# Kernel tuning notes

Hardware: AMD Instinct MI355X
Metric: run time of the kernel (lower is better)

Reference implementation:

```python
import jax, jax.numpy as jnp
import numpy as np

NUM_HEADS = 8  # from init_kwargs

def _conv1x1(x, W, b):
    # x: [B, Cin, H, W], W: [Cout, Cin], b: [Cout]  (nn.Conv2d kernel_size=1)
    return jnp.einsum('bchw,oc->bohw', x, W) + b[None, :, None, None]

def setup_inputs() -> dict:
    key = jax.random.key(0)
    ks = jax.random.split(key, 9)
    B, C, H, W = 8, 256, 32, 32
    Ck, Cv, Co = 256, 256, 256
    s = 1.0 / np.sqrt(C)
    return {
        'x':  jax.random.normal(ks[0], (B, C, H, W), dtype=jnp.float32),
        'Wq': jax.random.normal(ks[1], (Ck, C), dtype=jnp.float32) * s,
        'bq': jax.random.normal(ks[2], (Ck,), dtype=jnp.float32) * 0.02,
        'Wk': jax.random.normal(ks[3], (Ck, C), dtype=jnp.float32) * s,
        'bk': jax.random.normal(ks[4], (Ck,), dtype=jnp.float32) * 0.02,
        'Wv': jax.random.normal(ks[5], (Cv, C), dtype=jnp.float32) * s,
        'bv': jax.random.normal(ks[6], (Cv,), dtype=jnp.float32) * 0.02,
        'Wo': jax.random.normal(ks[7], (Co, Cv), dtype=jnp.float32) * s,
        'bo': jax.random.normal(ks[8], (Co,), dtype=jnp.float32) * 0.02,
    }

def reference(x, Wq, bq, Wk, bk, Wv, bv, Wo, bo):
    B, C, H, W = x.shape
    q = _conv1x1(x, Wq, bq)  # [B, Ck, H, W]
    k = _conv1x1(x, Wk, bk)  # [B, Ck, H, W]
    v = _conv1x1(x, Wv, bv)  # [B, Cv, H, W]
    nh = NUM_HEADS
    dk = q.shape[1] // nh
    dv = v.shape[1] // nh
    N = H * W
    # split heads, flatten spatial dims into sequence
    q = q.reshape(B, nh, dk, N) * (dk ** -0.5)
    k = k.reshape(B, nh, dk, N)
    v = v.reshape(B, nh, dv, N)
    logits = jnp.einsum('bhdn,bhdm->bhnm', q, k)        # [B, nh, N, N]
    attn = jax.nn.softmax(logits, axis=-1)
    o = jnp.einsum('bhnm,bhdm->bhdn', attn, v)           # [B, nh, dv, N]
    o = o.reshape(B, nh * dv, H, W)
    return _conv1x1(o, Wo, bo)                           # [B, Co, H, W]
```

## Files before the change

kernel.cpp:

```cpp
#include <hip/hip_runtime.h>
#include <math.h>

typedef unsigned short u16;
typedef __attribute__((ext_vector_type(8))) unsigned short u16x8;
typedef __attribute__((ext_vector_type(8))) short s16x8;
typedef __attribute__((ext_vector_type(4))) float f32x4;

#define QK_SCALE (0.17677669529663687f * 1.4426950408889634f)

__device__ __forceinline__ unsigned cvt2(float lo, float hi) {
  unsigned r;
  asm("v_cvt_pk_bf16_f32 %0, %1, %2" : "=v"(r) : "v"(lo), "v"(hi));
  return r;
}
__device__ __forceinline__ u16 f2bf(float f) { return (u16)cvt2(f, f); }
__device__ __forceinline__ u16x8 ld16(const void* p) { u16x8 v; __builtin_memcpy(&v, p, 16); return v; }
__device__ __forceinline__ void st16(void* p, u16x8 v) { __builtin_memcpy(p, &v, 16); }
__device__ __forceinline__ void st16s(void* p, s16x8 v) { __builtin_memcpy(p, &v, 16); }
__device__ __forceinline__ void st4(void* p, unsigned v) { __builtin_memcpy(p, &v, 4); }
__device__ __forceinline__ f32x4 ldf4(const void* p) { f32x4 v; __builtin_memcpy(&v, p, 16); return v; }
__device__ __forceinline__ void stf4(void* p, f32x4 v) { __builtin_memcpy(p, &v, 16); }
__device__ __forceinline__ s16x8 frag16(const void* p) { s16x8 v; __builtin_memcpy(&v, p, 16); return v; }
__device__ __forceinline__ s16x8 pack8(f32x4 lo, f32x4 hi) {
  union { unsigned u[4]; s16x8 s; } c;
  c.u[0] = cvt2(lo.x, lo.y); c.u[1] = cvt2(lo.z, lo.w);
  c.u[2] = cvt2(hi.x, hi.y); c.u[3] = cvt2(hi.z, hi.w);
  return c.s;
}

__global__ __launch_bounds__(256) void r19_qkv(
    const float* __restrict__ x,
    const float* __restrict__ Wq, const float* __restrict__ bq,
    const float* __restrict__ Wk, const float* __restrict__ bk,
    const float* __restrict__ Wv, const float* __restrict__ bv,
    u16* __restrict__ qo, u16* __restrict__ ko, u16* __restrict__ vo)
{
  __shared__ u16 xt[64][264];
  __shared__ u16 wlds[192][40];

  const int t = threadIdx.x;
  const int ntile = blockIdx.x, hp = blockIdx.y, b = blockIdx.z;
  const int n0 = ntile * 64, h0 = hp * 2;
  const int w = t >> 6, lane = t & 63, l15 = lane & 15, quad = lane >> 4;

  {
    const float* xrow = x + ((size_t)b * 256 + t) * 1024 + n0;
#pragma unroll
    for (int i = 0; i < 64; i += 4) {
      const f32x4 a = ldf4(xrow + i);
      xt[i + 0][t] = f2bf(a.x); xt[i + 1][t] = f2bf(a.y);
      xt[i + 2][t] = f2bf(a.z); xt[i + 3][t] = f2bf(a.w);
    }
  }

  f32x4 acc[12];
#pragma unroll
  for (int i = 0; i < 12; ++i) acc[i] = (f32x4){0.f, 0.f, 0.f, 0.f};

  for (int ks = 0; ks < 8; ++ks) {
    __syncthreads();
    if (t < 192) {
      const int m = t >> 6, hh = (t >> 5) & 1, r = t & 31;
      const float* M = (m == 0) ? Wq : (m == 1) ? Wk : Wv;
      const float* src = M + (size_t)((h0 + hh) * 32 + r) * 256 + ks * 32;
      st16s(&wlds[t][0],  pack8(ldf4(src),      ldf4(src + 4)));
      st16s(&wlds[t][8],  pack8(ldf4(src + 8),  ldf4(src + 12)));
      st16s(&wlds[t][16], pack8(ldf4(src + 16), ldf4(src + 20)));
      st16s(&wlds[t][24], pack8(ldf4(src + 24), ldf4(src + 28)));
    }
    __syncthreads();

    const s16x8 bfrag = frag16(&xt[w * 16 + l15][ks * 32 + quad * 8]);
#pragma unroll
    for (int mt = 0; mt < 12; ++mt) {
      const s16x8 af = frag16(&wlds[mt * 16 + l15][quad * 8]);
      acc[mt] = __builtin_amdgcn_mfma_f32_16x16x32_bf16(af, bfrag, acc[mt], 0, 0, 0);
    }
  }

  const int n = n0 + w * 16 + l15;
  const int sig = n & 127;
  const int ntn = sig >> 4, q4 = (sig >> 2) & 3, rn = sig & 3;
  const int nperm = (n & ~127) | ((ntn >> 1) << 5) | (q4 << 3) | ((ntn & 1) << 2) | rn;
#pragma unroll
  for (int hh = 0; hh < 2; ++hh) {
    const int h = h0 + hh;
    const size_t bh = (size_t)(b * 8 + h);
    u16* qrow = qo + (bh * 1024 + n) * 32;
    u16* krow = ko + (bh * 1024 + n) * 32;
#pragma unroll
    for (int half = 0; half < 2; ++half) {
      const int d0 = half * 16 + quad * 4;
      const f32x4 aq = acc[hh * 2 + half];
      const f32x4 ak = acc[4 + hh * 2 + half];
      const f32x4 av = acc[8 + hh * 2 + half];
      st4(qrow + d0,     cvt2((aq.x + bq[h * 32 + d0 + 0]) * QK_SCALE,
                              (aq.y + bq[h * 32 + d0 + 1]) * QK_SCALE));
      st4(qrow + d0 + 2, cvt2((aq.z + bq[h * 32 + d0 + 2]) * QK_SCALE,
                              (aq.w + bq[h * 32 + d0 + 3]) * QK_SCALE));
      st4(krow + d0,     cvt2(ak.x + bk[h * 32 + d0 + 0],
                              ak.y + bk[h * 32 + d0 + 1]));
      st4(krow + d0 + 2, cvt2(ak.z + bk[h * 32 + d0 + 2],
                              ak.w + bk[h * 32 + d0 + 3]));
#pragma unroll
      for (int rr = 0; rr < 4; ++rr) {
        const int d = d0 + rr;
        vo[(bh * 32 + d) * 1024 + nperm] = f2bf(av[rr] + bv[h * 32 + d]);
      }
    }
  }
}

__global__ __launch_bounds__(256) void r19_attn(
    const u16* __restrict__ qw, const u16* __restrict__ kw,
    const u16* __restrict__ vw, float* __restrict__ out)
{
  __shared__ u16 klds[128][40];
  __shared__ u16 vlds[32][136];

  const int t = threadIdx.x;
  const int qtile = blockIdx.x;
  const int bh = blockIdx.y;
  const int w = t >> 6, lane = t & 63, l15 = lane & 15, quad = lane >> 4;

  const s16x8 qfrag = frag16(
      qw + ((size_t)bh * 1024 + qtile * 64 + w * 16 + l15) * 32 + quad * 8);

  const u16* kbase = kw + ((size_t)bh * 1024 + (t >> 1)) * 32 + (t & 1) * 16;
  const u16* vbase = vw + ((size_t)bh * 32 + (t >> 3)) * 1024 + (t & 7) * 16;

  u16x8 gk0 = ld16(kbase), gk1 = ld16(kbase + 8);
  u16x8 gv0 = ld16(vbase), gv1 = ld16(vbase + 8);

  f32x4 o0 = {0.f, 0.f, 0.f, 0.f}, o1 = {0.f, 0.f, 0.f, 0.f};
  float mrun = -1e30f, lrun = 0.f;

  for (int kb = 0; kb < 8; ++kb) {
    if (kb) __syncthreads();
    st16(&klds[t >> 1][(t & 1) * 16], gk0);
    st16(&klds[t >> 1][(t & 1) * 16 + 8], gk1);
    st16(&vlds[t >> 3][(t & 7) * 16], gv0);
    st16(&vlds[t >> 3][(t & 7) * 16 + 8], gv1);
    if (kb < 7) {
      const u16* kn = kbase + (size_t)(kb + 1) * (128 * 32);
      const u16* vn = vbase + (size_t)(kb + 1) * 128;
      gk0 = ld16(kn); gk1 = ld16(kn + 8);
      gv0 = ld16(vn); gv1 = ld16(vn + 8);
    }
    __syncthreads();

    f32x4 s[8];
    const f32x4 zz = {0.f, 0.f, 0.f, 0.f};
#pragma unroll
    for (int nt2 = 0; nt2 < 8; ++nt2) {
      const s16x8 kf = frag16(&klds[nt2 * 16 + l15][quad * 8]);
      s[nt2] = __builtin_amdgcn_mfma_f32_16x16x32_bf16(kf, qfrag, zz, 0, 0, 0);
    }

    float mx = fmaxf(fmaxf(s[0][0], s[0][1]), fmaxf(s[0][2], s[0][3]));
#pragma unroll
    for (int nt2 = 1; nt2 < 8; ++nt2)
      mx = fmaxf(mx, fmaxf(fmaxf(s[nt2][0], s[nt2][1]),
                           fmaxf(s[nt2][2], s[nt2][3])));
    mx = fmaxf(mx, __shfl_xor(mx, 16));
    mx = fmaxf(mx, __shfl_xor(mx, 32));
    const float mnew = fmaxf(mrun, mx);
    const float alpha = exp2f(mrun - mnew);
    float rs = 0.f;
#pragma unroll
    for (int nt2 = 0; nt2 < 8; ++nt2) {
#pragma unroll
      for (int r = 0; r < 4; ++r) {
        s[nt2][r] = exp2f(s[nt2][r] - mnew);
        rs += s[nt2][r];
      }
    }
    rs += __shfl_xor(rs, 16);
    rs += __shfl_xor(rs, 32);
    lrun = lrun * alpha + rs;
    mrun = mnew;
#pragma unroll
    for (int r = 0; r < 4; ++r) { o0[r] *= alpha; o1[r] *= alpha; }

#pragma unroll
    for (int ks = 0; ks < 4; ++ks) {
      const s16x8 pf  = pack8(s[2 * ks], s[2 * ks + 1]);
      const s16x8 vf0 = frag16(&vlds[l15][ks * 32 + quad * 8]);
      const s16x8 vf1 = frag16(&vlds[16 + l15][ks * 32 + quad * 8]);
      o0 = __builtin_amdgcn_mfma_f32_16x16x32_bf16(vf0, pf, o0, 0, 0, 0);
      o1 = __builtin_amdgcn_mfma_f32_16x16x32_bf16(vf1, pf, o1, 0, 0, 0);
    }
  }

  const float inv = 1.0f / lrun;
  const int b = bh >> 3, hh = bh & 7;
  float* obase = out + ((size_t)b * 256 + hh * 32) * 1024
               + qtile * 64 + w * 16 + l15;
#pragma unroll
  for (int r = 0; r < 4; ++r) {
    obase[(size_t)(quad * 4 + r) * 1024]      = o0[r] * inv;
    obase[(size_t)(16 + quad * 4 + r) * 1024] = o1[r] * inv;
  }
}

__global__ __launch_bounds__(256) void r19_oproj(
    const float* __restrict__ Wo, const float* __restrict__ bo,
    float* __restrict__ out)
{
  __shared__ u16 o2t[32][264];
  const int t = threadIdx.x;
  const int nt = blockIdx.x, b = blockIdx.y;
  const int w = t >> 6, lane = t & 63, l15 = lane & 15, quad = lane >> 4;

  {
    const float* src = out + ((size_t)b * 256 + t) * 1024 + nt * 32;
#pragma unroll
    for (int i = 0; i < 32; i += 4) {
      const f32x4 a = ldf4(src + i);
      o2t[i + 0][t] = f2bf(a.x); o2t[i + 1][t] = f2bf(a.y);
      o2t[i + 2][t] = f2bf(a.z); o2t[i + 3][t] = f2bf(a.w);
    }
  }
  __syncthreads();

  f32x4 acc[4][2];
#pragma unroll
  for (int mt = 0; mt < 4; ++mt) {
    acc[mt][0] = (f32x4){0.f, 0.f, 0.f, 0.f};
    acc[mt][1] = (f32x4){0.f, 0.f, 0.f, 0.f};
  }

  for (int ks = 0; ks < 8; ++ks) {
    const s16x8 b0 = frag16(&o2t[l15][ks * 32 + quad * 8]);
    const s16x8 b1 = frag16(&o2t[16 + l15][ks * 32 + quad * 8]);
#pragma unroll
    for (int mt = 0; mt < 4; ++mt) {
      const float* wsrc = Wo + (size_t)(w * 64 + mt * 16 + l15) * 256 + ks * 32 + quad * 8;
      const s16x8 af = pack8(ldf4(wsrc), ldf4(wsrc + 4));
      acc[mt][0] = __builtin_amdgcn_mfma_f32_16x16x32_bf16(af, b0, acc[mt][0], 0, 0, 0);
      acc[mt][1] = __builtin_amdgcn_mfma_f32_16x16x32_bf16(af, b1, acc[mt][1], 0, 0, 0);
    }
  }

#pragma unroll
  for (int mt = 0; mt < 4; ++mt) {
#pragma unroll
    for (int r = 0; r < 4; ++r) {
      const int oc = w * 64 + mt * 16 + quad * 4 + r;
      const float bov = bo[oc];
      out[((size_t)b * 256 + oc) * 1024 + nt * 32 + l15]      = acc[mt][0][r] + bov;
      out[((size_t)b * 256 + oc) * 1024 + nt * 32 + 16 + l15] = acc[mt][1][r] + bov;
    }
  }
}

extern "C" void kernel_launch(void* const* d_in, const int* in_sizes, int n_in,
                              void* d_out, int out_size, void* d_ws, size_t ws_size,
                              hipStream_t stream) {
  (void)in_sizes; (void)n_in; (void)out_size; (void)ws_size;
  const float* x  = (const float*)d_in[0];
  const float* Wq = (const float*)d_in[1];
  const float* bq = (const float*)d_in[2];
  const float* Wk = (const float*)d_in[3];
  const float* bk = (const float*)d_in[4];
  const float* Wv = (const float*)d_in[5];
  const float* bv = (const float*)d_in[6];
  const float* Wo = (const float*)d_in[7];
  const float* bo = (const float*)d_in[8];
  float* out = (float*)d_out;

  char* ws = (char*)d_ws;
  u16* qw = (u16*)(ws);
  u16* kw = (u16*)(ws + (4u << 20));
  u16* vw = (u16*)(ws + (8u << 20));

  r19_qkv<<<dim3(16, 4, 8), 256, 0, stream>>>(
      x, Wq, bq, Wk, bk, Wv, bv, qw, kw, vw);
  r19_attn<<<dim3(16, 64), 256, 0, stream>>>(qw, kw, vw, out);
  r19_oproj<<<dim3(32, 8), 256, 0, stream>>>(Wo, bo, out);
}
```

Before: 137.5 us.

## Split keys across warps in attention and merge partial softmax via LDS

Restructures the attention kernel so each warp processes all 64 queries of the tile over its own quarter of the keys, reading K and V fragments directly from global memory instead of staging them through LDS with per-tile barriers. Partial max, sum and output accumulators are then combined across warps through shared memory. This is meant to remove the LDS staging and synchronisation overhead and to reuse each K/V fragment across four query tiles. In exchange it raises register usage and relies on cache-served direct global fragment loads.

Result: slower. 178.1 us (+29.6%).

```diff
diff --git a/kernel.cpp b/kernel.cpp
--- a/kernel.cpp
+++ b/kernel.cpp
@@ -28,7 +28,7 @@
   return c.s;
 }
 
-__global__ __launch_bounds__(256) void r19_qkv(
+__global__ __launch_bounds__(256) void r21_qkv(
     const float* __restrict__ x,
     const float* __restrict__ Wq, const float* __restrict__ bq,
     const float* __restrict__ Wk, const float* __restrict__ bk,
@@ -91,7 +91,7 @@
 #pragma unroll
     for (int half = 0; half < 2; ++half) {
       const int d0 = half * 16 + quad * 4;
-      const f32x4 aq = acc[hh * 2 + half];
+      const f32x4 aq = acc[0 + hh * 2 + half];
       const f32x4 ak = acc[4 + hh * 2 + half];
       const f32x4 av = acc[8 + hh * 2 + half];
       st4(qrow + d0,     cvt2((aq.x + bq[h * 32 + d0 + 0]) * QK_SCALE,
@@ -111,99 +111,135 @@
   }
 }
 
-__global__ __launch_bounds__(256) void r19_attn(
+__global__ __launch_bounds__(256) void r21_attn(
     const u16* __restrict__ qw, const u16* __restrict__ kw,
     const u16* __restrict__ vw, float* __restrict__ out)
 {
-  __shared__ u16 klds[128][40];
-  __shared__ u16 vlds[32][136];
+  __shared__ float olds[4][64][36];
+  __shared__ float mlm[4][4][16];
+  __shared__ float mll[4][4][16];
 
   const int t = threadIdx.x;
   const int qtile = blockIdx.x;
   const int bh = blockIdx.y;
   const int w = t >> 6, lane = t & 63, l15 = lane & 15, quad = lane >> 4;
 
-  const s16x8 qfrag = frag16(
-      qw + ((size_t)bh * 1024 + qtile * 64 + w * 16 + l15) * 32 + quad * 8);
-
-  const u16* kbase = kw + ((size_t)bh * 1024 + (t >> 1)) * 32 + (t & 1) * 16;
-  const u16* vbase = vw + ((size_t)bh * 32 + (t >> 3)) * 1024 + (t & 7) * 16;
-
-  u16x8 gk0 = ld16(kbase), gk1 = ld16(kbase + 8);
-  u16x8 gv0 = ld16(vbase), gv1 = ld16(vbase + 8);
-
-  f32x4 o0 = {0.f, 0.f, 0.f, 0.f}, o1 = {0.f, 0.f, 0.f, 0.f};
-  float mrun = -1e30f, lrun = 0.f;
-
-  for (int kb = 0; kb < 8; ++kb) {
-    if (kb) __syncthreads();
-    st16(&klds[t >> 1][(t & 1) * 16], gk0);
-    st16(&klds[t >> 1][(t & 1) * 16 + 8], gk1);
-    st16(&vlds[t >> 3][(t & 7) * 16], gv0);
-    st16(&vlds[t >> 3][(t & 7) * 16 + 8], gv1);
-    if (kb < 7) {
-      const u16* kn = kbase + (size_t)(kb + 1) * (128 * 32);
-      const u16* vn = vbase + (size_t)(kb + 1) * 128;
-      gk0 = ld16(kn); gk1 = ld16(kn + 8);
-      gv0 = ld16(vn); gv1 = ld16(vn + 8);
-    }
-    __syncthreads();
-
-    f32x4 s[8];
-    const f32x4 zz = {0.f, 0.f, 0.f, 0.f};
-#pragma unroll
-    for (int nt2 = 0; nt2 < 8; ++nt2) {
-      const s16x8 kf = frag16(&klds[nt2 * 16 + l15][quad * 8]);
-      s[nt2] = __builtin_amdgcn_mfma_f32_16x16x32_bf16(kf, qfrag, zz, 0, 0, 0);
-    }
-
-    float mx = fmaxf(fmaxf(s[0][0], s[0][1]), fmaxf(s[0][2], s[0][3]));
-#pragma unroll
-    for (int nt2 = 1; nt2 < 8; ++nt2)
-      mx = fmaxf(mx, fmaxf(fmaxf(s[nt2][0], s[nt2][1]),
-                           fmaxf(s[nt2][2], s[nt2][3])));
-    mx = fmaxf(mx, __shfl_xor(mx, 16));
-    mx = fmaxf(mx, __shfl_xor(mx, 32));
-    const float mnew = fmaxf(mrun, mx);
-    const float alpha = exp2f(mrun - mnew);
-    float rs = 0.f;
-#pragma unroll
-    for (int nt2 = 0; nt2 < 8; ++nt2) {
-#pragma unroll
-      for (int r = 0; r < 4; ++r) {
-        s[nt2][r] = exp2f(s[nt2][r] - mnew);
-        rs += s[nt2][r];
+  s16x8 qfrag[4];
+#pragma unroll
+  for (int qs = 0; qs < 4; ++qs)
+    qfrag[qs] = frag16(
+        qw + ((size_t)bh * 1024 + qtile * 64 + qs * 16 + l15) * 32 + quad * 8);
+
+  const u16* kwb = kw + (size_t)bh * 1024 * 32;
+  const u16* vwb = vw + (size_t)bh * 32 * 1024;
+
+  f32x4 o[4][2];
+#pragma unroll
+  for (int qs = 0; qs < 4; ++qs) {
+    o[qs][0] = (f32x4){0.f, 0.f, 0.f, 0.f};
+    o[qs][1] = (f32x4){0.f, 0.f, 0.f, 0.f};
+  }
+  float m[4] = {-1e30f, -1e30f, -1e30f, -1e30f};
+  float l[4] = {0.f, 0.f, 0.f, 0.f};
+
+  const f32x4 zz = {0.f, 0.f, 0.f, 0.f};
+#pragma unroll
+  for (int c = 0; c < 4; ++c) {
+    const int cb = w * 64 + c * 256;
+    const u16* kp = kwb + (size_t)cb * 32;
+    const u16* vp = vwb + cb;
+
+    f32x4 s[4][4];
+#pragma unroll
+    for (int kt = 0; kt < 4; ++kt) {
+      const s16x8 kf = frag16(kp + (size_t)(kt * 16 + l15) * 32 + quad * 8);
+#pragma unroll
+      for (int qs = 0; qs < 4; ++qs)
+        s[qs][kt] = __builtin_amdgcn_mfma_f32_16x16x32_bf16(kf, qfrag[qs], zz, 0, 0, 0);
+    }
+
+#pragma unroll
+    for (int qs = 0; qs < 4; ++qs) {
+      float mx = fmaxf(fmaxf(s[qs][0][0], s[qs][0][1]),
+                       fmaxf(s[qs][0][2], s[qs][0][3]));
+#pragma unroll
+      for (int kt = 1; kt < 4; ++kt)
+        mx = fmaxf(mx, fmaxf(fmaxf(s[qs][kt][0], s[qs][kt][1]),
+                             fmaxf(s[qs][kt][2], s[qs][kt][3])));
+      mx = fmaxf(mx, __shfl_xor(mx, 16));
+      mx = fmaxf(mx, __shfl_xor(mx, 32));
+      const float mnew = fmaxf(m[qs], mx);
+      const float al = exp2f(m[qs] - mnew);
+      float rs = 0.f;
+#pragma unroll
+      for (int kt = 0; kt < 4; ++kt) {
+#pragma unroll
+        for (int r = 0; r < 4; ++r) {
+          s[qs][kt][r] = exp2f(s[qs][kt][r] - mnew);
+          rs += s[qs][kt][r];
+        }
       }
-    }
-    rs += __shfl_xor(rs, 16);
-    rs += __shfl_xor(rs, 32);
-    lrun = lrun * alpha + rs;
-    mrun = mnew;
-#pragma unroll
-    for (int r = 0; r < 4; ++r) { o0[r] *= alpha; o1[r] *= alpha; }
-
-#pragma unroll
-    for (int ks = 0; ks < 4; ++ks) {
-      const s16x8 pf  = pack8(s[2 * ks], s[2 * ks + 1]);
-      const s16x8 vf0 = frag16(&vlds[l15][ks * 32 + quad * 8]);
-      const s16x8 vf1 = frag16(&vlds[16 + l15][ks * 32 + quad * 8]);
-      o0 = __builtin_amdgcn_mfma_f32_16x16x32_bf16(vf0, pf, o0, 0, 0, 0);
-      o1 = __builtin_amdgcn_mfma_f32_16x16x32_bf16(vf1, pf, o1, 0, 0, 0);
-    }
-  }
-
-  const float inv = 1.0f / lrun;
+      rs += __shfl_xor(rs, 16);
+      rs += __shfl_xor(rs, 32);
+      l[qs] = l[qs] * al + rs;
+      m[qs] = mnew;
+#pragma unroll
+      for (int r = 0; r < 4; ++r) { o[qs][0][r] *= al; o[qs][1][r] *= al; }
+    }
+
+#pragma unroll
+    for (int ks2 = 0; ks2 < 2; ++ks2) {
+      const s16x8 vf0 = frag16(vp + (size_t)l15 * 1024 + ks2 * 32 + quad * 8);
+      const s16x8 vf1 = frag16(vp + (size_t)(16 + l15) * 1024 + ks2 * 32 + quad * 8);
+#pragma unroll
+      for (int qs = 0; qs < 4; ++qs) {
+        const s16x8 pf = pack8(s[qs][2 * ks2], s[qs][2 * ks2 + 1]);
+        o[qs][0] = __builtin_amdgcn_mfma_f32_16x16x32_bf16(vf0, pf, o[qs][0], 0, 0, 0);
+        o[qs][1] = __builtin_amdgcn_mfma_f32_16x16x32_bf16(vf1, pf, o[qs][1], 0, 0, 0);
+      }
+    }
+  }
+
+  mlm[w][quad][l15] = m[quad];
+  mll[w][quad][l15] = l[quad];
+  __syncthreads();
+#pragma unroll
+  for (int qs = 0; qs < 4; ++qs) {
+    float mv0 = mlm[0][qs][l15], mv1 = mlm[1][qs][l15];
+    float mv2 = mlm[2][qs][l15], mv3 = mlm[3][qs][l15];
+    const float M = fmaxf(fmaxf(mv0, mv1), fmaxf(mv2, mv3));
+    const float L = exp2f(mv0 - M) * mll[0][qs][l15]
+                  + exp2f(mv1 - M) * mll[1][qs][l15]
+                  + exp2f(mv2 - M) * mll[2][qs][l15]
+                  + exp2f(mv3 - M) * mll[3][qs][l15];
+    const float sc = exp2f(m[qs] - M) / L;
+    f32x4 a0, a1;
+#pragma unroll
+    for (int r = 0; r < 4; ++r) { a0[r] = o[qs][0][r] * sc; a1[r] = o[qs][1][r] * sc; }
+    stf4(&olds[w][qs * 16 + l15][quad * 4], a0);
+    stf4(&olds[w][qs * 16 + l15][16 + quad * 4], a1);
+  }
+  __syncthreads();
+
+  f32x4 r0 = {0.f, 0.f, 0.f, 0.f}, r1 = {0.f, 0.f, 0.f, 0.f};
+#pragma unroll
+  for (int wv = 0; wv < 4; ++wv) {
+    const f32x4 p0 = ldf4(&olds[wv][w * 16 + l15][quad * 4]);
+    const f32x4 p1 = ldf4(&olds[wv][w * 16 + l15][16 + quad * 4]);
+#pragma unroll
+    for (int r = 0; r < 4; ++r) { r0[r] += p0[r]; r1[r] += p1[r]; }
+  }
   const int b = bh >> 3, hh = bh & 7;
   float* obase = out + ((size_t)b * 256 + hh * 32) * 1024
                + qtile * 64 + w * 16 + l15;
 #pragma unroll
   for (int r = 0; r < 4; ++r) {
-    obase[(size_t)(quad * 4 + r) * 1024]      = o0[r] * inv;
-    obase[(size_t)(16 + quad * 4 + r) * 1024] = o1[r] * inv;
-  }
-}
-
-__global__ __launch_bounds__(256) void r19_oproj(
+    obase[(size_t)(quad * 4 + r) * 1024]      = r0[r];
+    obase[(size_t)(16 + quad * 4 + r) * 1024] = r1[r];
+  }
+}
+
+__global__ __launch_bounds__(256) void r21_oproj(
     const float* __restrict__ Wo, const float* __restrict__ bo,
     float* __restrict__ out)
 {
@@ -274,8 +310,8 @@
   u16* kw = (u16*)(ws + (4u << 20));
   u16* vw = (u16*)(ws + (8u << 20));
 
-  r19_qkv<<<dim3(16, 4, 8), 256, 0, stream>>>(
+  r21_qkv<<<dim3(16, 4, 8), 256, 0, stream>>>(
       x, Wq, bq, Wk, bk, Wv, bv, qw, kw, vw);
-  r19_attn<<<dim3(16, 64), 256, 0, stream>>>(qw, kw, vw, out);
-  r19_oproj<<<dim3(32, 8), 256, 0, stream>>>(Wo, bo, out);
-}
+  r21_attn<<<dim3(16, 64), 256, 0, stream>>>(qw, kw, vw, out);
+  r21_oproj<<<dim3(32, 8), 256, 0, stream>>>(Wo, bo, out);
+}
```

## Coalesce x/W staging loads, swizzle LDS, double-buffer Wo in oproj

Applied to the files above, without the earlier changes.

The QKV and output-projection kernels now load activations and weights with coalesced lanes, where each thread previously walked its own row. The transposed bf16 tiles in LDS use an XOR swizzle to avoid bank conflicts. In the output projection, Wo is staged into double-buffered LDS instead of being read and converted from global memory separately by each wave. This cuts strided global traffic and duplicated weight loads, at the cost of more LDS use (lower occupancy) and an extra barrier per k-step.

New measurement: 132.4 us. 3.7% less time.

```diff
diff --git a/kernel.cpp b/kernel.cpp
--- a/kernel.cpp
+++ b/kernel.cpp
@@ -18,6 +18,10 @@
 __device__ __forceinline__ void st16(void* p, u16x8 v) { __builtin_memcpy(p, &v, 16); }
 __device__ __forceinline__ void st16s(void* p, s16x8 v) { __builtin_memcpy(p, &v, 16); }
 __device__ __forceinline__ void st4(void* p, unsigned v) { __builtin_memcpy(p, &v, 4); }
+__device__ __forceinline__ void st8(void* p, unsigned lo, unsigned hi) {
+  unsigned long long v = ((unsigned long long)hi << 32) | (unsigned long long)lo;
+  __builtin_memcpy(p, &v, 8);
+}
 __device__ __forceinline__ f32x4 ldf4(const void* p) { f32x4 v; __builtin_memcpy(&v, p, 16); return v; }
 __device__ __forceinline__ void stf4(void* p, f32x4 v) { __builtin_memcpy(p, &v, 16); }
 __device__ __forceinline__ s16x8 frag16(const void* p) { s16x8 v; __builtin_memcpy(&v, p, 16); return v; }
@@ -28,7 +32,7 @@
   return c.s;
 }
 
-__global__ __launch_bounds__(256) void r19_qkv(
+__global__ __launch_bounds__(256) void r22_qkv(
     const float* __restrict__ x,
     const float* __restrict__ Wq, const float* __restrict__ bq,
     const float* __restrict__ Wk, const float* __restrict__ bk,
@@ -42,14 +46,19 @@
   const int ntile = blockIdx.x, hp = blockIdx.y, b = blockIdx.z;
   const int n0 = ntile * 64, h0 = hp * 2;
   const int w = t >> 6, lane = t & 63, l15 = lane & 15, quad = lane >> 4;
+  const int oct = t & 7;
 
   {
-    const float* xrow = x + ((size_t)b * 256 + t) * 1024 + n0;
-#pragma unroll
-    for (int i = 0; i < 64; i += 4) {
-      const f32x4 a = ldf4(xrow + i);
-      xt[i + 0][t] = f2bf(a.x); xt[i + 1][t] = f2bf(a.y);
-      xt[i + 2][t] = f2bf(a.z); xt[i + 3][t] = f2bf(a.w);
+    const int i = t & 15, co = t >> 4;
+    const float* xb = x + ((size_t)b * 256 + co) * 1024 + n0 + i * 4;
+    const int msk = (i & 7) << 3;
+#pragma unroll
+    for (int p = 0; p < 16; ++p) {
+      const f32x4 a = ldf4(xb + (size_t)p * 16 * 1024);
+      const int c = p * 16 + co;
+#pragma unroll
+      for (int j = 0; j < 4; ++j)
+        xt[i * 4 + j][(c ^ msk)] = f2bf(a[j]);
     }
   }
 
@@ -59,18 +68,22 @@
 
   for (int ks = 0; ks < 8; ++ks) {
     __syncthreads();
-    if (t < 192) {
-      const int m = t >> 6, hh = (t >> 5) & 1, r = t & 31;
-      const float* M = (m == 0) ? Wq : (m == 1) ? Wk : Wv;
-      const float* src = M + (size_t)((h0 + hh) * 32 + r) * 256 + ks * 32;
-      st16s(&wlds[t][0],  pack8(ldf4(src),      ldf4(src + 4)));
-      st16s(&wlds[t][8],  pack8(ldf4(src + 8),  ldf4(src + 12)));
-      st16s(&wlds[t][16], pack8(ldf4(src + 16), ldf4(src + 20)));
-      st16s(&wlds[t][24], pack8(ldf4(src + 24), ldf4(src + 28)));
+    {
+#pragma unroll
+      for (int u = 0; u < 6; ++u) {
+        const int row = (u * 256 + t) >> 3;
+        const int m = row >> 6, hh = (row >> 5) & 1, rr = row & 31;
+        const float* M = (m == 0) ? Wq : (m == 1) ? Wk : Wv;
+        const f32x4 a = ldf4(M + (size_t)((h0 + hh) * 32 + rr) * 256
+                             + ks * 32 + oct * 4);
+        st8(&wlds[row][oct * 4], cvt2(a.x, a.y), cvt2(a.z, a.w));
+      }
     }
     __syncthreads();
 
-    const s16x8 bfrag = frag16(&xt[w * 16 + l15][ks * 32 + quad * 8]);
+    const int nrow = w * 16 + l15;
+    const s16x8 bfrag = frag16(
+        &xt[nrow][(ks * 32 + quad * 8) ^ (((nrow >> 2) & 7) << 3)]);
 #pragma unroll
     for (int mt = 0; mt < 12; ++mt) {
       const s16x8 af = frag16(&wlds[mt * 16 + l15][quad * 8]);
@@ -91,7 +104,7 @@
 #pragma unroll
     for (int half = 0; half < 2; ++half) {
       const int d0 = half * 16 + quad * 4;
-      const f32x4 aq = acc[hh * 2 + half];
+      const f32x4 aq = acc[0 + hh * 2 + half];
       const f32x4 ak = acc[4 + hh * 2 + half];
       const f32x4 av = acc[8 + hh * 2 + half];
       st4(qrow + d0,     cvt2((aq.x + bq[h * 32 + d0 + 0]) * QK_SCALE,
@@ -111,7 +124,7 @@
   }
 }
 
-__global__ __launch_bounds__(256) void r19_attn(
+__global__ __launch_bounds__(256) void r22_attn(
     const u16* __restrict__ qw, const u16* __restrict__ kw,
     const u16* __restrict__ vw, float* __restrict__ out)
 {
@@ -203,24 +216,42 @@
   }
 }
 
-__global__ __launch_bounds__(256) void r19_oproj(
+__global__ __launch_bounds__(256) void r22_oproj(
     const float* __restrict__ Wo, const float* __restrict__ bo,
     float* __restrict__ out)
 {
   __shared__ u16 o2t[32][264];
+  __shared__ u16 wl3[2][256][40];
+
   const int t = threadIdx.x;
   const int nt = blockIdx.x, b = blockIdx.y;
   const int w = t >> 6, lane = t & 63, l15 = lane & 15, quad = lane >> 4;
+  const int oct = t & 7;
 
   {
-    const float* src = out + ((size_t)b * 256 + t) * 1024 + nt * 32;
-#pragma unroll
-    for (int i = 0; i < 32; i += 4) {
-      const f32x4 a = ldf4(src + i);
-      o2t[i + 0][t] = f2bf(a.x); o2t[i + 1][t] = f2bf(a.y);
-      o2t[i + 2][t] = f2bf(a.z); o2t[i + 3][t] = f2bf(a.w);
-    }
-  }
+    const int co = t >> 3;
+    const float* ob = out + ((size_t)b * 256 + co) * 1024 + nt * 32 + oct * 4;
+    const int msk = oct << 3;
+#pragma unroll
+    for (int p = 0; p < 8; ++p) {
+      const f32x4 a = ldf4(ob + (size_t)p * 32 * 1024);
+      const int c = p * 32 + co;
+#pragma unroll
+      for (int j = 0; j < 4; ++j)
+        o2t[oct * 4 + j][(c ^ msk)] = f2bf(a[j]);
+    }
+  }
+
+  auto stage_wo = [&](int ks, int buf) {
+#pragma unroll
+    for (int u = 0; u < 8; ++u) {
+      const int row = u * 32 + (t >> 3);
+      const f32x4 a = ldf4(Wo + (size_t)row * 256 + ks * 32 + oct * 4);
+      st8(&wl3[buf][row][oct * 4], cvt2(a.x, a.y), cvt2(a.z, a.w));
+    }
+  };
+
+  stage_wo(0, 0);
   __syncthreads();
 
   f32x4 acc[4][2];
@@ -231,15 +262,18 @@
   }
 
   for (int ks = 0; ks < 8; ++ks) {
-    const s16x8 b0 = frag16(&o2t[l15][ks * 32 + quad * 8]);
-    const s16x8 b1 = frag16(&o2t[16 + l15][ks * 32 + quad * 8]);
+    if (ks < 7) stage_wo(ks + 1, (ks + 1) & 1);
+    const s16x8 b0 = frag16(
+        &o2t[l15][(ks * 32 + quad * 8) ^ (((l15 >> 2) & 7) << 3)]);
+    const s16x8 b1 = frag16(
+        &o2t[16 + l15][(ks * 32 + quad * 8) ^ ((((16 + l15) >> 2) & 7) << 3)]);
 #pragma unroll
     for (int mt = 0; mt < 4; ++mt) {
-      const float* wsrc = Wo + (size_t)(w * 64 + mt * 16 + l15) * 256 + ks * 32 + quad * 8;
-      const s16x8 af = pack8(ldf4(wsrc), ldf4(wsrc + 4));
+      const s16x8 af = frag16(&wl3[ks & 1][w * 64 + mt * 16 + l15][quad * 8]);
       acc[mt][0] = __builtin_amdgcn_mfma_f32_16x16x32_bf16(af, b0, acc[mt][0], 0, 0, 0);
       acc[mt][1] = __builtin_amdgcn_mfma_f32_16x16x32_bf16(af, b1, acc[mt][1], 0, 0, 0);
     }
+    __syncthreads();
   }
 
 #pragma unroll
@@ -274,8 +308,8 @@
   u16* kw = (u16*)(ws + (4u << 20));
   u16* vw = (u16*)(ws + (8u << 20));
 
-  r19_qkv<<<dim3(16, 4, 8), 256, 0, stream>>>(
+  r22_qkv<<<dim3(16, 4, 8), 256, 0, stream>>>(
       x, Wq, bq, Wk, bk, Wv, bv, qw, kw, vw);
-  r19_attn<<<dim3(16, 64), 256, 0, stream>>>(qw, kw, vw, out);
-  r19_oproj<<<dim3(32, 8), 256, 0, stream>>>(Wo, bo, out);
-}
+  r22_attn<<<dim3(16, 64), 256, 0, stream>>>(qw, kw, vw, out);
+  r22_oproj<<<dim3(32, 8), 256, 0, stream>>>(Wo, bo, out);
+}
```
